# Kernel optimization log

Measured on AMD Instinct MI355X. Metric: run time of the kernel, lower is better.

Reference implementation:

```python
import jax, jax.numpy as jnp
import numpy as np

N_NODES = 50000
N_EDGES = 800000
N_GRAPHS = 64
NEG_SLOPE = 0.01  # nn.LeakyReLU default


def setup_inputs() -> dict:
    key = jax.random.key(0)
    ks = jax.random.split(key, 10)
    x = jax.random.normal(ks[0], (N_NODES, 128), dtype=jnp.float32)
    edge_index = jax.random.randint(ks[1], (2, N_EDGES), 0, N_NODES, dtype=jnp.int32)
    # balanced, sorted graph assignment -> every one of the 64 graphs is non-empty
    batch = ((jnp.arange(N_NODES, dtype=jnp.int32) * N_GRAPHS) // N_NODES).astype(jnp.int32)

    def lin(k, fan_in, fan_out):
        lim = 1.0 / np.sqrt(fan_in)
        return jax.random.uniform(k, (fan_in, fan_out), jnp.float32, -lim, lim)

    return {
        "x": x, "edge_index": edge_index, "batch": batch,
        "W1": lin(ks[2], 128, 64),   "b1": jnp.zeros((64,), jnp.float32),
        "W2": lin(ks[3], 64, 128),   "b2": jnp.zeros((128,), jnp.float32),
        "W3": lin(ks[4], 128, 256),  "b3": jnp.zeros((256,), jnp.float32),
        "Wc1": lin(ks[5], 256, 1024), "bc1": jnp.zeros((1024,), jnp.float32),
        "Wc2": lin(ks[6], 1024, 512), "bc2": jnp.zeros((512,), jnp.float32),
        "Wc3": lin(ks[7], 512, 4),    "bc3": jnp.zeros((4,), jnp.float32),
    }


def _gcn_conv(x, W, b, src, dst, dinv, n):
    """PyG GCNConv: add self-loops, sym-normalize, X W then scatter-add."""
    h = x @ W                                   # [N, out]
    norm = (dinv[src] * dinv[dst])[:, None]     # per-edge coefficient
    out = jax.ops.segment_sum(h[src] * norm, dst, num_segments=n)
    out = out + h * (dinv * dinv)[:, None]      # self-loop contribution
    return out + b


def reference(x, edge_index, batch, W1, b1, W2, b2, W3, b3,
              Wc1, bc1, Wc2, bc2, Wc3, bc3):
    n = x.shape[0]
    src, dst = edge_index[0], edge_index[1]
    # degrees with self-loops (edge weights = 1); shared by all three convs
    deg = jnp.zeros((n,), x.dtype).at[dst].add(1.0) + 1.0
    dinv = jax.lax.rsqrt(deg)

    leaky = lambda v: jnp.where(v >= 0, v, NEG_SLOPE * v)

    h = leaky(_gcn_conv(x, W1, b1, src, dst, dinv, n))   # [N, 64]
    h = leaky(_gcn_conv(h, W2, b2, src, dst, dinv, n))   # [N, 128]
    h = _gcn_conv(h, W3, b3, src, dst, dinv, n)          # [N, 256]

    g = jax.ops.segment_max(h, batch, num_segments=N_GRAPHS)  # [G, 256]

    g = jax.nn.relu(g @ Wc1 + bc1)
    g = jax.nn.relu(g @ Wc2 + bc2)
    return g @ Wc3 + bc3                                  # [G, 4]
```

## Files before the change

### kernel.cpp

```cpp
#include <hip/hip_runtime.h>
#include <math.h>

#define NN 50000
#define NE 800000
#define NG 64
#define NEG 0.01f

__device__ __forceinline__ unsigned fenc(float f) {
  unsigned b = __float_as_uint(f);
  return (b & 0x80000000u) ? ~b : (b | 0x80000000u);
}
__device__ __forceinline__ float fdec(unsigned k) {
  unsigned b = (k & 0x80000000u) ? (k ^ 0x80000000u) : ~k;
  return __uint_as_float(b);
}

__global__ void hist_kernel(const int* __restrict__ dst, int* __restrict__ cnt) {
  int i = blockIdx.x * blockDim.x + threadIdx.x;
  if (i < NE) atomicAdd(&cnt[dst[i]], 1);
}

#define SCAN_ELE 512
#define SCAN_NB ((NN + SCAN_ELE - 1) / SCAN_ELE)

__global__ __launch_bounds__(256) void scan_reduce(const int* __restrict__ cnt,
                                                   int* __restrict__ partials) {
  int b = blockIdx.x, t = threadIdx.x;
  int i = b * SCAN_ELE + t * 2;
  int v0 = (i < NN) ? cnt[i] : 0;
  int v1 = (i + 1 < NN) ? cnt[i + 1] : 0;
  __shared__ int red[256];
  red[t] = v0 + v1;
  __syncthreads();
  for (int ofs = 128; ofs > 0; ofs >>= 1) {
    if (t < ofs) red[t] += red[t + ofs];
    __syncthreads();
  }
  if (t == 0) partials[b] = red[0];
}

__global__ void scan_partials(int* __restrict__ partials) {
  __shared__ int s[128];
  int t = threadIdx.x;
  int v = (t < SCAN_NB) ? partials[t] : 0;
  s[t] = v;
  __syncthreads();
  for (int ofs = 1; ofs < 128; ofs <<= 1) {
    int u = (t >= ofs) ? s[t - ofs] : 0;
    __syncthreads();
    s[t] += u;
    __syncthreads();
  }
  if (t < SCAN_NB) partials[t] = s[t] - v;
}

__global__ __launch_bounds__(256) void scan_write(const int* __restrict__ cnt,
                                                  const int* __restrict__ partials,
                                                  int* __restrict__ row_start,
                                                  int* __restrict__ cursor,
                                                  float* __restrict__ dinv) {
  int b = blockIdx.x, t = threadIdx.x;
  int i = b * SCAN_ELE + t * 2;
  int v0 = (i < NN) ? cnt[i] : 0;
  int v1 = (i + 1 < NN) ? cnt[i + 1] : 0;
  int s = v0 + v1;
  __shared__ int sc[256];
  sc[t] = s;
  __syncthreads();
  for (int ofs = 1; ofs < 256; ofs <<= 1) {
    int u = (t >= ofs) ? sc[t - ofs] : 0;
    __syncthreads();
    sc[t] += u;
    __syncthreads();
  }
  int base = partials[b] + sc[t] - s;
  if (i < NN) {
    row_start[i] = base; cursor[i] = base;
    dinv[i] = 1.0f / sqrtf((float)(v0 + 1));
  }
  if (i + 1 < NN) {
    row_start[i + 1] = base + v0; cursor[i + 1] = base + v0;
    dinv[i + 1] = 1.0f / sqrtf((float)(v1 + 1));
  }
  if (b == SCAN_NB - 1 && t == 255) row_start[NN] = partials[b] + sc[255];
}

__global__ void scatter_kernel(const int* __restrict__ src, const int* __restrict__ dst,
                               int* __restrict__ cursor, int* __restrict__ csr) {
  int i = blockIdx.x * blockDim.x + threadIdx.x;
  if (i < NE) {
    int d = dst[i];
    int pos = atomicAdd(&cursor[d], 1);
    csr[pos] = src[i];
  }
}

template <int BN, int MODE>
__global__ __launch_bounds__(256) void gemm_big(const float* __restrict__ A,
                                                const float* __restrict__ B,
                                                const float* __restrict__ bias,
                                                const float* __restrict__ dinv,
                                                float* __restrict__ C,
                                                int M, int N, int K) {
  constexpr int TN = BN / 16;
  __shared__ float As[16][132];
  __shared__ float Bs[16][BN];
  const int t = threadIdx.x;
  const int tx = t & 15, ty = t >> 4;
  const int bm = blockIdx.y * 128, bn = blockIdx.x * BN;
  const int ar = t >> 2, ac = (t & 3) * 4;
  const int r0 = bm + ar, r1 = r0 + 64;
  const bool ok0 = r0 < M, ok1 = r1 < M;
  float acc[8][TN] = {};
  for (int k0 = 0; k0 < K; k0 += 16) {
    float4 a0 = ok0 ? *(const float4*)(A + (size_t)r0 * K + k0 + ac) : make_float4(0.f,0.f,0.f,0.f);
    float4 a1 = ok1 ? *(const float4*)(A + (size_t)r1 * K + k0 + ac) : make_float4(0.f,0.f,0.f,0.f);
    float4 bv0, bv1;
    if (BN == 128) {
      const int kr = t >> 5, c4 = (t & 31) * 4;
      bv0 = *(const float4*)(B + (size_t)(k0 + kr) * N + bn + c4);
      bv1 = *(const float4*)(B + (size_t)(k0 + kr + 8) * N + bn + c4);
    } else {
      const int kr = t >> 4, c4 = (t & 15) * 4;
      bv0 = *(const float4*)(B + (size_t)(k0 + kr) * N + bn + c4);
      bv1 = make_float4(0.f,0.f,0.f,0.f);
    }
    __syncthreads();
    As[ac + 0][ar] = a0.x; As[ac + 1][ar] = a0.y; As[ac + 2][ar] = a0.z; As[ac + 3][ar] = a0.w;
    As[ac + 0][ar + 64] = a1.x; As[ac + 1][ar + 64] = a1.y;
    As[ac + 2][ar + 64] = a1.z; As[ac + 3][ar + 64] = a1.w;
    if (BN == 128) {
      *(float4*)&Bs[t >> 5][(t & 31) * 4] = bv0;
      *(float4*)&Bs[(t >> 5) + 8][(t & 31) * 4] = bv1;
    } else {
      *(float4*)&Bs[t >> 4][(t & 15) * 4] = bv0;
    }
    __syncthreads();
#pragma unroll
    for (int k = 0; k < 16; ++k) {
      float a[8], b[TN];
      *(float4*)&a[0] = *(const float4*)&As[k][ty * 8];
      *(float4*)&a[4] = *(const float4*)&As[k][ty * 8 + 4];
      *(float4*)&b[0] = *(const float4*)&Bs[k][tx * 4];
      if (TN == 8) *(float4*)&b[4] = *(const float4*)&Bs[k][64 + tx * 4];
#pragma unroll
      for (int i = 0; i < 8; ++i)
#pragma unroll
        for (int j = 0; j < TN; ++j) acc[i][j] = fmaf(a[i], b[j], acc[i][j]);
    }
  }
  float bb[TN];
#pragma unroll
  for (int j = 0; j < TN; ++j) bb[j] = 0.f;
  if (MODE >= 1) {
#pragma unroll
    for (int j = 0; j < 4; ++j) bb[j] = bias[bn + tx * 4 + j];
    if (TN == 8)
#pragma unroll
      for (int j = 0; j < 4; ++j) bb[4 + j] = bias[bn + 64 + tx * 4 + j];
  }
#pragma unroll
  for (int i = 0; i < 8; ++i) {
    const int r = bm + ty * 8 + i;
    if (r < M) {
      const float dn = (MODE <= 1) ? dinv[r] : 1.0f;
      float v[TN];
#pragma unroll
      for (int j = 0; j < TN; ++j) {
        float u = acc[i][j] + bb[j];
        if (MODE == 1) u = (u >= 0.f) ? u : NEG * u;
        if (MODE <= 1) u = u * dn;
        v[j] = u;
      }
      *(float4*)(C + (size_t)r * N + bn + tx * 4) = make_float4(v[0], v[1], v[2], v[3]);
      if (TN == 8)
        *(float4*)(C + (size_t)r * N + bn + 64 + tx * 4) = make_float4(v[4], v[5], v[6], v[7]);
    }
  }
}

template <int MODE>
__global__ __launch_bounds__(256) void agg64_kernel(const float* __restrict__ hs,
                                                    const float* __restrict__ dinv,
                                                    const int* __restrict__ row_start,
                                                    const int* __restrict__ csr,
                                                    const float* __restrict__ bias,
                                                    float* __restrict__ out) {
  int wid = (blockIdx.x * 256 + threadIdx.x) >> 6;
  int lane = threadIdx.x & 63;
  if (wid >= NN) return;
  int e0 = row_start[wid], e1 = row_start[wid + 1];
  float a0 = 0.f, a1 = 0.f, a2 = 0.f, a3 = 0.f;
  int e = e0;
  for (; e + 4 <= e1; e += 4) {
    int s0 = csr[e], s1 = csr[e + 1], s2 = csr[e + 2], s3 = csr[e + 3];
    a0 += hs[(size_t)s0 * 64 + lane];
    a1 += hs[(size_t)s1 * 64 + lane];
    a2 += hs[(size_t)s2 * 64 + lane];
    a3 += hs[(size_t)s3 * 64 + lane];
  }
  for (; e < e1; ++e) a0 += hs[(size_t)csr[e] * 64 + lane];
  float dn = dinv[wid];
  float acc = (a0 + a1) + (a2 + a3) + hs[(size_t)wid * 64 + lane];
  float v = dn * acc;
  if (MODE == 1) {
    v += bias[lane];
    v = (v >= 0.f) ? v : NEG * v;
    v *= dn;
  }
  out[(size_t)wid * 64 + lane] = v;
}

__global__ __launch_bounds__(256) void agg128_kernel(const float* __restrict__ hs,
                                                     const float* __restrict__ dinv,
                                                     const int* __restrict__ row_start,
                                                     const int* __restrict__ csr,
                                                     float* __restrict__ out) {
  int wid = (blockIdx.x * 256 + threadIdx.x) >> 6;
  int lane = threadIdx.x & 63;
  if (wid >= NN) return;
  const float2* h2 = (const float2*)hs;
  int e0 = row_start[wid], e1 = row_start[wid + 1];
  float x0 = 0.f, y0 = 0.f, x1 = 0.f, y1 = 0.f, x2 = 0.f, y2 = 0.f, x3 = 0.f, y3 = 0.f;
  int e = e0;
  for (; e + 4 <= e1; e += 4) {
    int s0 = csr[e], s1 = csr[e + 1], s2 = csr[e + 2], s3 = csr[e + 3];
    float2 v0 = h2[(size_t)s0 * 64 + lane];
    float2 v1 = h2[(size_t)s1 * 64 + lane];
    float2 v2 = h2[(size_t)s2 * 64 + lane];
    float2 v3 = h2[(size_t)s3 * 64 + lane];
    x0 += v0.x; y0 += v0.y; x1 += v1.x; y1 += v1.y;
    x2 += v2.x; y2 += v2.y; x3 += v3.x; y3 += v3.y;
  }
  for (; e < e1; ++e) {
    float2 v = h2[(size_t)csr[e] * 64 + lane];
    x0 += v.x; y0 += v.y;
  }
  float2 self = h2[(size_t)wid * 64 + lane];
  float dn = dinv[wid];
  float2 o;
  o.x = dn * ((x0 + x1) + (x2 + x3) + self.x);
  o.y = dn * ((y0 + y1) + (y2 + y3) + self.y);
  ((float2*)out)[(size_t)wid * 64 + lane] = o;
}

#define SEG_CHUNK 125
__global__ __launch_bounds__(256) void segmax_kernel(const float* __restrict__ h,
                                                     const int* __restrict__ batch,
                                                     unsigned* __restrict__ gmax) {
  int t = threadIdx.x;
  int n0 = blockIdx.x * SEG_CHUNK;
  int n1 = n0 + SEG_CHUNK; if (n1 > NN) n1 = NN;
  int cur = batch[n0];
  float m = -INFINITY;
  for (int n = n0; n < n1; ++n) {
    int g = batch[n];
    if (g != cur) {
      atomicMax(&gmax[cur * 256 + t], fenc(m));
      cur = g;
      m = -INFINITY;
    }
    m = fmaxf(m, h[(size_t)n * 256 + t]);
  }
  atomicMax(&gmax[cur * 256 + t], fenc(m));
}

__global__ __launch_bounds__(256) void mlp_kernel(const unsigned* __restrict__ gmax,
                                                  const float* __restrict__ Wc1,
                                                  const float* __restrict__ bc1,
                                                  const float* __restrict__ Wc2,
                                                  const float* __restrict__ bc2,
                                                  const float* __restrict__ Wc3,
                                                  const float* __restrict__ bc3,
                                                  float* __restrict__ out) {
  __shared__ float g0[256];
  __shared__ float h1[1024];
  __shared__ float h2[512];
  __shared__ float red[256][4];
  const int b = blockIdx.x, t = threadIdx.x;

  g0[t] = fdec(gmax[b * 256 + t]);
  __syncthreads();

  {
    float4 acc = *(const float4*)(bc1 + 4 * t);
#pragma unroll 8
    for (int k = 0; k < 256; ++k) {
      float gv = g0[k];
      float4 w = *(const float4*)(Wc1 + (size_t)k * 1024 + 4 * t);
      acc.x = fmaf(gv, w.x, acc.x);
      acc.y = fmaf(gv, w.y, acc.y);
      acc.z = fmaf(gv, w.z, acc.z);
      acc.w = fmaf(gv, w.w, acc.w);
    }
    h1[4 * t + 0] = fmaxf(acc.x, 0.f);
    h1[4 * t + 1] = fmaxf(acc.y, 0.f);
    h1[4 * t + 2] = fmaxf(acc.z, 0.f);
    h1[4 * t + 3] = fmaxf(acc.w, 0.f);
  }
  __syncthreads();

  {
    float2 acc = *(const float2*)(bc2 + 2 * t);
#pragma unroll 8
    for (int k = 0; k < 1024; ++k) {
      float hv = h1[k];
      float2 w = *(const float2*)(Wc2 + (size_t)k * 512 + 2 * t);
      acc.x = fmaf(hv, w.x, acc.x);
      acc.y = fmaf(hv, w.y, acc.y);
    }
    h2[2 * t + 0] = fmaxf(acc.x, 0.f);
    h2[2 * t + 1] = fmaxf(acc.y, 0.f);
  }
  __syncthreads();

  float acc[4] = {0.f, 0.f, 0.f, 0.f};
  for (int k = t; k < 512; k += 256) {
    float hv = h2[k];
#pragma unroll
    for (int n = 0; n < 4; ++n) acc[n] = fmaf(hv, Wc3[k * 4 + n], acc[n]);
  }
#pragma unroll
  for (int n = 0; n < 4; ++n) red[t][n] = acc[n];
  __syncthreads();
  for (int s = 128; s > 0; s >>= 1) {
    if (t < s)
#pragma unroll
      for (int n = 0; n < 4; ++n) red[t][n] += red[t + s][n];
    __syncthreads();
  }
  if (t < 4) out[b * 4 + t] = red[0][t] + bc3[t];
}

extern "C" void kernel_launch(void* const* d_in, const int* in_sizes, int n_in,
                              void* d_out, int out_size, void* d_ws, size_t ws_size,
                              hipStream_t stream) {
  const float* x   = (const float*)d_in[0];
  const int*   ei  = (const int*)d_in[1];
  const int* batch = (const int*)d_in[2];
  const float* W1  = (const float*)d_in[3];
  const float* b1  = (const float*)d_in[4];
  const float* W2  = (const float*)d_in[5];
  const float* b2  = (const float*)d_in[6];
  const float* W3  = (const float*)d_in[7];
  const float* b3  = (const float*)d_in[8];
  const float* Wc1 = (const float*)d_in[9];
  const float* bc1 = (const float*)d_in[10];
  const float* Wc2 = (const float*)d_in[11];
  const float* bc2 = (const float*)d_in[12];
  const float* Wc3 = (const float*)d_in[13];
  const float* bc3 = (const float*)d_in[14];
  const int* src = ei;
  const int* dst = ei + NE;

  char* base = (char*)d_ws;
  size_t off = 0;
  auto take = [&](size_t bytes) {
    size_t o = off;
    off += (bytes + 255) & ~(size_t)255;
    return o;
  };
  int*      deg_cnt   = (int*)(base + take((size_t)NN * 4));
  float*    dinv      = (float*)(base + take((size_t)NN * 4));
  int*      row_start = (int*)(base + take((size_t)(NN + 1) * 4));
  int*      cursor    = (int*)(base + take((size_t)NN * 4));
  int*      partials  = (int*)(base + take((size_t)SCAN_NB * 4));
  int*      csr       = (int*)(base + take((size_t)NE * 4));
  unsigned* gmax      = (unsigned*)(base + take((size_t)NG * 256 * 4));
  float* B64_a  = (float*)(base + take((size_t)NN * 64 * 4));
  float* B64_b  = (float*)(base + take((size_t)NN * 64 * 4));
  float* B128_a = (float*)(base + take((size_t)NN * 128 * 4));
  float* B128_b = (float*)(base + take((size_t)NN * 128 * 4));
  float* out3   = B64_a;

  hipMemsetAsync(deg_cnt, 0, (size_t)NN * 4, stream);
  hipMemsetAsync(gmax, 0, (size_t)NG * 256 * 4, stream);
  hist_kernel<<<(NE + 255) / 256, 256, 0, stream>>>(dst, deg_cnt);
  scan_reduce<<<SCAN_NB, 256, 0, stream>>>(deg_cnt, partials);
  scan_partials<<<1, 128, 0, stream>>>(partials);
  scan_write<<<SCAN_NB, 256, 0, stream>>>(deg_cnt, partials, row_start, cursor, dinv);
  scatter_kernel<<<(NE + 255) / 256, 256, 0, stream>>>(src, dst, cursor, csr);

  const int gy = (NN + 127) / 128;

  gemm_big<64, 0><<<dim3(1, gy), 256, 0, stream>>>(x, W1, nullptr, dinv, B64_a, NN, 64, 128);
  agg64_kernel<1><<<(NN * 64) / 256, 256, 0, stream>>>(B64_a, dinv, row_start, csr, b1, B64_b);

  agg64_kernel<0><<<(NN * 64) / 256, 256, 0, stream>>>(B64_b, dinv, row_start, csr, nullptr, B64_a);
  gemm_big<128, 1><<<dim3(1, gy), 256, 0, stream>>>(B64_a, W2, b2, dinv, B128_a, NN, 128, 64);

  agg128_kernel<<<(NN * 64) / 256, 256, 0, stream>>>(B128_a, dinv, row_start, csr, B128_b);
  gemm_big<128, 2><<<dim3(2, gy), 256, 0, stream>>>(B128_b, W3, b3, nullptr, out3, NN, 256, 128);

  segmax_kernel<<<(NN + SEG_CHUNK - 1) / SEG_CHUNK, 256, 0, stream>>>(out3, batch, gmax);
  mlp_kernel<<<NG, 256, 0, stream>>>(gmax, Wc1, bc1, Wc2, bc2, Wc3, bc3, (float*)d_out);
}
```

Baseline: 510.9 us.

## Split classifier MLP into three kernels with more blocks and split-K atomics

The single per-graph MLP kernel (64 blocks) is split into three launches. Layer 1 uses 4 column blocks per graph, layer 2 uses split-K over 4 chunks and 2 column halves with atomicAdd into a zeroed buffer, and layer 3 applies the bias and ReLU and then the final projection. This spreads the dense work across far more CUs. It adds two kernel launches, a memset, global round-trips for intermediates, and nondeterministic float atomic summation order.

Measured after the change: 475.6 us. 1.07x faster.

```diff
diff --git a/kernel.cpp b/kernel.cpp
--- a/kernel.cpp
+++ b/kernel.cpp
@@ -265,58 +265,50 @@
   atomicMax(&gmax[cur * 256 + t], fenc(m));
 }
 
-__global__ __launch_bounds__(256) void mlp_kernel(const unsigned* __restrict__ gmax,
-                                                  const float* __restrict__ Wc1,
-                                                  const float* __restrict__ bc1,
-                                                  const float* __restrict__ Wc2,
-                                                  const float* __restrict__ bc2,
-                                                  const float* __restrict__ Wc3,
-                                                  const float* __restrict__ bc3,
-                                                  float* __restrict__ out) {
+__global__ __launch_bounds__(256) void mlp_l1(const unsigned* __restrict__ gmax,
+                                              const float* __restrict__ Wc1,
+                                              const float* __restrict__ bc1,
+                                              float* __restrict__ c1) {
+  const int g = blockIdx.x >> 2;
+  const int c = (blockIdx.x & 3) * 256 + threadIdx.x;
   __shared__ float g0[256];
-  __shared__ float h1[1024];
-  __shared__ float h2[512];
+  g0[threadIdx.x] = fdec(gmax[g * 256 + threadIdx.x]);
+  __syncthreads();
+  float acc = bc1[c];
+#pragma unroll 16
+  for (int k = 0; k < 256; ++k)
+    acc = fmaf(g0[k], Wc1[(size_t)k * 1024 + c], acc);
+  c1[g * 1024 + c] = fmaxf(acc, 0.f);
+}
+
+__global__ __launch_bounds__(256) void mlp_l2(const float* __restrict__ c1,
+                                              const float* __restrict__ Wc2,
+                                              float* __restrict__ c2raw) {
+  const int b = blockIdx.x;
+  const int g = b >> 3;
+  const int cc = (b >> 2) & 1;
+  const int kc = b & 3;
+  const int c = cc * 256 + threadIdx.x;
+  __shared__ float h[256];
+  h[threadIdx.x] = c1[g * 1024 + kc * 256 + threadIdx.x];
+  __syncthreads();
+  float acc = 0.f;
+#pragma unroll 16
+  for (int k = 0; k < 256; ++k)
+    acc = fmaf(h[k], Wc2[(size_t)(kc * 256 + k) * 512 + c], acc);
+  atomicAdd(&c2raw[g * 512 + c], acc);
+}
+
+__global__ __launch_bounds__(256) void mlp_l3(const float* __restrict__ c2raw,
+                                              const float* __restrict__ bc2,
+                                              const float* __restrict__ Wc3,
+                                              const float* __restrict__ bc3,
+                                              float* __restrict__ out) {
   __shared__ float red[256][4];
-  const int b = blockIdx.x, t = threadIdx.x;
-
-  g0[t] = fdec(gmax[b * 256 + t]);
-  __syncthreads();
-
-  {
-    float4 acc = *(const float4*)(bc1 + 4 * t);
-#pragma unroll 8
-    for (int k = 0; k < 256; ++k) {
-      float gv = g0[k];
-      float4 w = *(const float4*)(Wc1 + (size_t)k * 1024 + 4 * t);
-      acc.x = fmaf(gv, w.x, acc.x);
-      acc.y = fmaf(gv, w.y, acc.y);
-      acc.z = fmaf(gv, w.z, acc.z);
-      acc.w = fmaf(gv, w.w, acc.w);
-    }
-    h1[4 * t + 0] = fmaxf(acc.x, 0.f);
-    h1[4 * t + 1] = fmaxf(acc.y, 0.f);
-    h1[4 * t + 2] = fmaxf(acc.z, 0.f);
-    h1[4 * t + 3] = fmaxf(acc.w, 0.f);
-  }
-  __syncthreads();
-
-  {
-    float2 acc = *(const float2*)(bc2 + 2 * t);
-#pragma unroll 8
-    for (int k = 0; k < 1024; ++k) {
-      float hv = h1[k];
-      float2 w = *(const float2*)(Wc2 + (size_t)k * 512 + 2 * t);
-      acc.x = fmaf(hv, w.x, acc.x);
-      acc.y = fmaf(hv, w.y, acc.y);
-    }
-    h2[2 * t + 0] = fmaxf(acc.x, 0.f);
-    h2[2 * t + 1] = fmaxf(acc.y, 0.f);
-  }
-  __syncthreads();
-
+  const int m = blockIdx.x, t = threadIdx.x;
   float acc[4] = {0.f, 0.f, 0.f, 0.f};
   for (int k = t; k < 512; k += 256) {
-    float hv = h2[k];
+    float hv = fmaxf(c2raw[m * 512 + k] + bc2[k], 0.f);
 #pragma unroll
     for (int n = 0; n < 4; ++n) acc[n] = fmaf(hv, Wc3[k * 4 + n], acc[n]);
   }
@@ -329,7 +321,7 @@
       for (int n = 0; n < 4; ++n) red[t][n] += red[t + s][n];
     __syncthreads();
   }
-  if (t < 4) out[b * 4 + t] = red[0][t] + bc3[t];
+  if (t < 4) out[m * 4 + t] = red[0][t] + bc3[t];
 }
 
 extern "C" void kernel_launch(void* const* d_in, const int* in_sizes, int n_in,
@@ -367,6 +359,8 @@
   int*      partials  = (int*)(base + take((size_t)SCAN_NB * 4));
   int*      csr       = (int*)(base + take((size_t)NE * 4));
   unsigned* gmax      = (unsigned*)(base + take((size_t)NG * 256 * 4));
+  float*    c1buf     = (float*)(base + take((size_t)NG * 1024 * 4));
+  float*    c2raw     = (float*)(base + take((size_t)NG * 512 * 4));
   float* B64_a  = (float*)(base + take((size_t)NN * 64 * 4));
   float* B64_b  = (float*)(base + take((size_t)NN * 64 * 4));
   float* B128_a = (float*)(base + take((size_t)NN * 128 * 4));
@@ -375,6 +369,7 @@
 
   hipMemsetAsync(deg_cnt, 0, (size_t)NN * 4, stream);
   hipMemsetAsync(gmax, 0, (size_t)NG * 256 * 4, stream);
+  hipMemsetAsync(c2raw, 0, (size_t)NG * 512 * 4, stream);
   hist_kernel<<<(NE + 255) / 256, 256, 0, stream>>>(dst, deg_cnt);
   scan_reduce<<<SCAN_NB, 256, 0, stream>>>(deg_cnt, partials);
   scan_partials<<<1, 128, 0, stream>>>(partials);
@@ -393,5 +388,7 @@
   gemm_big<128, 2><<<dim3(2, gy), 256, 0, stream>>>(B128_b, W3, b3, nullptr, out3, NN, 256, 128);
 
   segmax_kernel<<<(NN + SEG_CHUNK - 1) / SEG_CHUNK, 256, 0, stream>>>(out3, batch, gmax);
-  mlp_kernel<<<NG, 256, 0, stream>>>(gmax, Wc1, bc1, Wc2, bc2, Wc3, bc3, (float*)d_out);
-}
+  mlp_l1<<<NG * 4, 256, 0, stream>>>(gmax, Wc1, bc1, c1buf);
+  mlp_l2<<<NG * 8, 256, 0, stream>>>(c1buf, Wc2, c2raw);
+  mlp_l3<<<NG, 256, 0, stream>>>(c2raw, bc2, Wc3, bc3, (float*)d_out);
+}
```
